# Performance work log

Hardware: AMD Instinct MI355X
Metric: run time of the kernel (lower is better)

The kernel has to match this reference:

```python
import jax, jax.numpy as jnp
import numpy as np

N = 100000
E = 1600000
F1 = 512
F3 = 128
H = 128
C = 64
SW = 0.2
FW = 1.0 - SW
BN_EPS = 1e-5


def setup_inputs() -> dict:
    key = jax.random.key(0)
    ks = jax.random.split(key, 12)
    def glorot(k, shape):
        lim = float(np.sqrt(6.0 / (shape[0] + shape[1])))
        return jax.random.uniform(k, shape, jnp.float32, -lim, lim)
    return {
        "x1": jax.random.normal(ks[0], (N, F1), jnp.float32),
        "x2": jax.random.normal(ks[1], (N, F3), jnp.float32),
        "edge_index": jax.random.randint(ks[2], (2, E), 0, N, jnp.int64),
        "W1": glorot(ks[3], (F1, H)), "b1": jnp.zeros((H,), jnp.float32),
        "W2": glorot(ks[4], (F3, H)), "b2": jnp.zeros((H,), jnp.float32),
        "Wg1": glorot(ks[5], (H, H)), "bg1": jnp.zeros((H,), jnp.float32),
        "Wg2": glorot(ks[6], (H, C)), "bg2": jnp.zeros((C,), jnp.float32),
        "gamma": jnp.ones((H,), jnp.float32), "beta": jnp.zeros((H,), jnp.float32),
        "rmean": jnp.zeros((H,), jnp.float32), "rvar": jnp.ones((H,), jnp.float32),
    }


def reference(x1, x2, edge_index, W1, b1, W2, b2, Wg1, bg1, Wg2, bg2, gamma, beta, rmean, rvar):
    # Embedding blend: fw * lin1(features) + sw * lin2(structural embedding)
    h = FW * (x1 @ W1 + b1) + SW * (x2 @ W2 + b2)  # [N, H]
    src, dst = edge_index[0], edge_index[1]
    # GCNConv layer 1 (normalize=False, add_self_loops=False): transform then scatter-add
    z = h @ Wg1                                              # [N, H]
    agg = jax.ops.segment_sum(z[src], dst, num_segments=N) + bg1  # [N, H]
    # BatchNorm1d (eval, running stats) + ReLU; dropout is identity in eval
    agg = (agg - rmean) * jax.lax.rsqrt(rvar + BN_EPS) * gamma + beta
    agg = jax.nn.relu(agg)
    # GCNConv layer 2 -> logits
    z2 = agg @ Wg2                                           # [N, C]
    out = jax.ops.segment_sum(z2[src], dst, num_segments=N) + bg2
    return out
```

## Files before the change

### kernel.cpp

```cpp
#include <hip/hip_runtime.h>
#include <hip/hip_fp16.h>
#include <cstddef>

#define NN    100000
#define EE    1600000
#define F1D   512
#define F3D   128
#define HD    128
#define CD    64
#define SWc   0.2f
#define FWc   0.8f
#define BN_EPS 1e-5f

#define SCAN_B 1024
#define NB ((NN + SCAN_B - 1) / SCAN_B)

typedef _Float16 half8 __attribute__((ext_vector_type(8)));
typedef float f32x4 __attribute__((ext_vector_type(4)));

__global__ __launch_bounds__(256) void count_kernel(
    const int* __restrict__ dst, int* __restrict__ deg)
{
    int e = blockIdx.x * 256 + threadIdx.x;
    if (e < EE) atomicAdd(&deg[dst[e]], 1);
}

__global__ __launch_bounds__(SCAN_B) void scan_partial_kernel(
    const int* __restrict__ deg, int* __restrict__ partials)
{
    __shared__ int sh[SCAN_B / 64];
    int i = blockIdx.x * SCAN_B + threadIdx.x;
    int v = (i < NN) ? deg[i] : 0;
#pragma unroll
    for (int d = 32; d > 0; d >>= 1) v += __shfl_down(v, d, 64);
    int lane = threadIdx.x & 63, wv = threadIdx.x >> 6;
    if (lane == 0) sh[wv] = v;
    __syncthreads();
    if (threadIdx.x < SCAN_B / 64) {
        int s = sh[threadIdx.x];
#pragma unroll
        for (int d = SCAN_B / 128; d > 0; d >>= 1) s += __shfl_down(s, d, 64);
        if (threadIdx.x == 0) partials[blockIdx.x] = s;
    }
}

__global__ __launch_bounds__(128) void scan_base_kernel(
    int* __restrict__ partials, int* __restrict__ offsets)
{
    __shared__ int sh[128];
    int t = threadIdx.x;
    int v = (t < NB) ? partials[t] : 0;
    sh[t] = v;
    __syncthreads();
    for (int d = 1; d < 128; d <<= 1) {
        int u = (t >= d) ? sh[t - d] : 0;
        __syncthreads();
        sh[t] += u;
        __syncthreads();
    }
    if (t < NB) partials[t] = sh[t] - v;
    if (t == NB - 1) offsets[NN] = sh[t];
}

__global__ __launch_bounds__(SCAN_B) void scan_apply_kernel(
    const int* __restrict__ deg, const int* __restrict__ partials,
    int* __restrict__ offsets, int* __restrict__ cursor)
{
    __shared__ int sh[SCAN_B];
    int t = threadIdx.x;
    int i = blockIdx.x * SCAN_B + t;
    int v = (i < NN) ? deg[i] : 0;
    sh[t] = v;
    __syncthreads();
    for (int d = 1; d < SCAN_B; d <<= 1) {
        int u = (t >= d) ? sh[t - d] : 0;
        __syncthreads();
        sh[t] += u;
        __syncthreads();
    }
    if (i < NN) {
        int excl = sh[t] - v + partials[blockIdx.x];
        offsets[i] = excl;
        cursor[i]  = excl;
    }
}

__global__ __launch_bounds__(256) void fill_kernel(
    const int* __restrict__ src, const int* __restrict__ dst,
    int* __restrict__ cursor, int* __restrict__ csr_src)
{
    int e = blockIdx.x * 256 + threadIdx.x;
    if (e < EE) {
        int d = dst[e];
        int pos = atomicAdd(&cursor[d], 1);
        csr_src[pos] = src[e];
    }
}

__global__ __launch_bounds__(256) void prep_kernel(
    const float* __restrict__ W1, const float* __restrict__ W2,
    const float* __restrict__ Wg1, const float* __restrict__ Wg2,
    const float* __restrict__ b1, const float* __restrict__ b2,
    _Float16* __restrict__ Wc_t, _Float16* __restrict__ Wg1_t,
    _Float16* __restrict__ Wg2_t, float* __restrict__ hbuf)
{
    int i = blockIdx.x * 256 + threadIdx.x;
    if (i < 128 * 640) {
        int n = i / 640, k = i % 640;
        float v = (k < F1D) ? FWc * W1[(size_t)k * HD + n]
                            : SWc * W2[(size_t)(k - F1D) * HD + n];
        Wc_t[i] = (_Float16)v;
    } else if (i < 128 * 640 + 128 * 128) {
        int j = i - 128 * 640; int n = j / 128, k = j % 128;
        Wg1_t[j] = (_Float16)Wg1[(size_t)k * HD + n];
    } else if (i < 128 * 640 + 128 * 128 + 64 * 128) {
        int j = i - 128 * 640 - 128 * 128; int n = j / 128, k = j % 128;
        Wg2_t[j] = (_Float16)Wg2[(size_t)k * CD + n];
    } else if (i < 128 * 640 + 128 * 128 + 64 * 128 + 128) {
        int j = i - (128 * 640 + 128 * 128 + 64 * 128);
        hbuf[j] = FWc * b1[j] + SWc * b2[j];
    }
}

__global__ __launch_bounds__(256) void gemm1_mfma(
    const float* __restrict__ x1, const float* __restrict__ x2,
    const _Float16* __restrict__ Wc_t, const _Float16* __restrict__ Wg1_t,
    const float* __restrict__ hbuf, _Float16* __restrict__ z)
{
    __shared__ __align__(16) _Float16 As[128][72];
    __shared__ __align__(16) _Float16 Bs[128][72];
    __shared__ __align__(16) _Float16 Hs[128][136];

    const int tid  = threadIdx.x;
    const int wave = tid >> 6;
    const int lane = tid & 63;
    const int quad = lane >> 4;
    const int l16  = lane & 15;
    const int row0 = blockIdx.x * 128;

    const int sr = tid >> 1;
    const int sc = (tid & 1) * 32;

    f32x4 acc[2][8];
    const f32x4 zero4 = {0.f, 0.f, 0.f, 0.f};
#pragma unroll
    for (int mi = 0; mi < 2; ++mi)
#pragma unroll
        for (int ni = 0; ni < 8; ++ni) acc[mi][ni] = zero4;

    for (int t = 0; t < 10; ++t) {
        const float* xp; int stride, kb;
        if (t < 8) { xp = x1; stride = F1D; kb = t * 64; }
        else       { xp = x2; stride = F3D; kb = (t - 8) * 64; }
        __syncthreads();
        {
            int gr = row0 + sr;
            if (gr < NN) {
                const float4* rp = (const float4*)(xp + (size_t)gr * stride + kb + sc);
#pragma unroll
                for (int i = 0; i < 4; ++i) {
                    float4 f0 = rp[2 * i];
                    float4 f1 = rp[2 * i + 1];
                    half8 hv = { (_Float16)f0.x, (_Float16)f0.y, (_Float16)f0.z, (_Float16)f0.w,
                                 (_Float16)f1.x, (_Float16)f1.y, (_Float16)f1.z, (_Float16)f1.w };
                    *(half8*)&As[sr][sc + i * 8] = hv;
                }
            } else {
                half8 zv = { (_Float16)0.f, (_Float16)0.f, (_Float16)0.f, (_Float16)0.f,
                             (_Float16)0.f, (_Float16)0.f, (_Float16)0.f, (_Float16)0.f };
#pragma unroll
                for (int i = 0; i < 4; ++i) *(half8*)&As[sr][sc + i * 8] = zv;
            }
            const _Float16* wp = Wc_t + (size_t)sr * 640 + t * 64 + sc;
#pragma unroll
            for (int i = 0; i < 4; ++i)
                *(half8*)&Bs[sr][sc + i * 8] = *(const half8*)(wp + i * 8);
        }
        __syncthreads();
#pragma unroll
        for (int ks = 0; ks < 2; ++ks) {
            half8 a[2], b[8];
#pragma unroll
            for (int mi = 0; mi < 2; ++mi)
                a[mi] = *(const half8*)&As[wave * 32 + mi * 16 + l16][ks * 32 + quad * 8];
#pragma unroll
            for (int ni = 0; ni < 8; ++ni)
                b[ni] = *(const half8*)&Bs[ni * 16 + l16][ks * 32 + quad * 8];
#pragma unroll
            for (int mi = 0; mi < 2; ++mi)
#pragma unroll
                for (int ni = 0; ni < 8; ++ni)
                    acc[mi][ni] = __builtin_amdgcn_mfma_f32_16x16x32_f16(
                        a[mi], b[ni], acc[mi][ni], 0, 0, 0);
        }
    }

    {
        float hbv[8];
#pragma unroll
        for (int ni = 0; ni < 8; ++ni) hbv[ni] = hbuf[ni * 16 + l16];
#pragma unroll
        for (int mi = 0; mi < 2; ++mi)
#pragma unroll
            for (int ni = 0; ni < 8; ++ni)
#pragma unroll
                for (int r = 0; r < 4; ++r)
                    Hs[wave * 32 + mi * 16 + quad * 4 + r][ni * 16 + l16] =
                        (_Float16)(acc[mi][ni][r] + hbv[ni]);
    }

#pragma unroll
    for (int mi = 0; mi < 2; ++mi)
#pragma unroll
        for (int ni = 0; ni < 8; ++ni) acc[mi][ni] = zero4;

    for (int t = 0; t < 2; ++t) {
        __syncthreads();
        {
            const _Float16* wp = Wg1_t + (size_t)sr * 128 + t * 64 + sc;
#pragma unroll
            for (int i = 0; i < 4; ++i)
                *(half8*)&Bs[sr][sc + i * 8] = *(const half8*)(wp + i * 8);
        }
        __syncthreads();
#pragma unroll
        for (int ks = 0; ks < 2; ++ks) {
            half8 a[2], b[8];
#pragma unroll
            for (int mi = 0; mi < 2; ++mi)
                a[mi] = *(const half8*)&Hs[wave * 32 + mi * 16 + l16][t * 64 + ks * 32 + quad * 8];
#pragma unroll
            for (int ni = 0; ni < 8; ++ni)
                b[ni] = *(const half8*)&Bs[ni * 16 + l16][ks * 32 + quad * 8];
#pragma unroll
            for (int mi = 0; mi < 2; ++mi)
#pragma unroll
                for (int ni = 0; ni < 8; ++ni)
                    acc[mi][ni] = __builtin_amdgcn_mfma_f32_16x16x32_f16(
                        a[mi], b[ni], acc[mi][ni], 0, 0, 0);
        }
    }

#pragma unroll
    for (int mi = 0; mi < 2; ++mi)
#pragma unroll
        for (int ni = 0; ni < 8; ++ni)
#pragma unroll
            for (int r = 0; r < 4; ++r)
                Hs[wave * 32 + mi * 16 + quad * 4 + r][ni * 16 + l16] =
                    (_Float16)acc[mi][ni][r];
    __syncthreads();
    {
        int gr = row0 + sr;
        if (gr < NN) {
            int c0 = (tid & 1) * 64;
            _Float16* zp = z + (size_t)gr * HD + c0;
#pragma unroll
            for (int i = 0; i < 8; ++i)
                *(half8*)(zp + i * 8) = *(const half8*)&Hs[sr][c0 + i * 8];
        }
    }
}

__global__ __launch_bounds__(256) void gemm2_mfma(
    const float* __restrict__ agg, const _Float16* __restrict__ Wg2_t,
    const float* __restrict__ bg1, const float* __restrict__ gamma,
    const float* __restrict__ beta, const float* __restrict__ rmean,
    const float* __restrict__ rvar, _Float16* __restrict__ z2)
{
    __shared__ __align__(16) _Float16 As[128][72];
    __shared__ __align__(16) _Float16 Bs[64][72];
    __shared__ float sS[HD], sT[HD];

    const int tid = threadIdx.x;
    if (tid < HD) {
        float s = gamma[tid] * rsqrtf(rvar[tid] + BN_EPS);
        sS[tid] = s;
        sT[tid] = (bg1[tid] - rmean[tid]) * s + beta[tid];
    }
    __syncthreads();

    const int wave = tid >> 6;
    const int lane = tid & 63;
    const int quad = lane >> 4;
    const int l16  = lane & 15;
    const int row0 = blockIdx.x * 128;
    const int sr = tid >> 1;
    const int sc = (tid & 1) * 32;

    f32x4 acc[2][4];
    const f32x4 zero4 = {0.f, 0.f, 0.f, 0.f};
#pragma unroll
    for (int mi = 0; mi < 2; ++mi)
#pragma unroll
        for (int ni = 0; ni < 4; ++ni) acc[mi][ni] = zero4;

    for (int t = 0; t < 2; ++t) {
        __syncthreads();
        {
            int gr = row0 + sr;
            if (gr < NN) {
                const float4* rp = (const float4*)(agg + (size_t)gr * HD + t * 64 + sc);
#pragma unroll
                for (int i = 0; i < 4; ++i) {
                    float4 f0 = rp[2 * i];
                    float4 f1 = rp[2 * i + 1];
                    int k = t * 64 + sc + i * 8;
                    float v0 = fmaxf(fmaf(f0.x, sS[k + 0], sT[k + 0]), 0.f);
                    float v1 = fmaxf(fmaf(f0.y, sS[k + 1], sT[k + 1]), 0.f);
                    float v2 = fmaxf(fmaf(f0.z, sS[k + 2], sT[k + 2]), 0.f);
                    float v3 = fmaxf(fmaf(f0.w, sS[k + 3], sT[k + 3]), 0.f);
                    float v4 = fmaxf(fmaf(f1.x, sS[k + 4], sT[k + 4]), 0.f);
                    float v5 = fmaxf(fmaf(f1.y, sS[k + 5], sT[k + 5]), 0.f);
                    float v6 = fmaxf(fmaf(f1.z, sS[k + 6], sT[k + 6]), 0.f);
                    float v7 = fmaxf(fmaf(f1.w, sS[k + 7], sT[k + 7]), 0.f);
                    half8 hv = { (_Float16)v0, (_Float16)v1, (_Float16)v2, (_Float16)v3,
                                 (_Float16)v4, (_Float16)v5, (_Float16)v6, (_Float16)v7 };
                    *(half8*)&As[sr][sc + i * 8] = hv;
                }
            } else {
                half8 zv = { (_Float16)0.f, (_Float16)0.f, (_Float16)0.f, (_Float16)0.f,
                             (_Float16)0.f, (_Float16)0.f, (_Float16)0.f, (_Float16)0.f };
#pragma unroll
                for (int i = 0; i < 4; ++i) *(half8*)&As[sr][sc + i * 8] = zv;
            }
            int n = tid >> 2, c = (tid & 3) * 16;
            const _Float16* wp = Wg2_t + (size_t)n * 128 + t * 64 + c;
            *(half8*)&Bs[n][c]     = *(const half8*)wp;
            *(half8*)&Bs[n][c + 8] = *(const half8*)(wp + 8);
        }
        __syncthreads();
#pragma unroll
        for (int ks = 0; ks < 2; ++ks) {
            half8 a[2], b[4];
#pragma unroll
            for (int mi = 0; mi < 2; ++mi)
                a[mi] = *(const half8*)&As[wave * 32 + mi * 16 + l16][ks * 32 + quad * 8];
#pragma unroll
            for (int ni = 0; ni < 4; ++ni)
                b[ni] = *(const half8*)&Bs[ni * 16 + l16][ks * 32 + quad * 8];
#pragma unroll
            for (int mi = 0; mi < 2; ++mi)
#pragma unroll
                for (int ni = 0; ni < 4; ++ni)
                    acc[mi][ni] = __builtin_amdgcn_mfma_f32_16x16x32_f16(
                        a[mi], b[ni], acc[mi][ni], 0, 0, 0);
        }
    }

    __syncthreads();
#pragma unroll
    for (int mi = 0; mi < 2; ++mi)
#pragma unroll
        for (int ni = 0; ni < 4; ++ni)
#pragma unroll
            for (int r = 0; r < 4; ++r)
                As[wave * 32 + mi * 16 + quad * 4 + r][ni * 16 + l16] =
                    (_Float16)acc[mi][ni][r];
    __syncthreads();
    {
        int gr = row0 + sr;
        if (gr < NN) {
            _Float16* zp = z2 + (size_t)gr * CD + sc;
            *(half8*)(zp)      = *(const half8*)&As[sr][sc];
            *(half8*)(zp + 8)  = *(const half8*)&As[sr][sc + 8];
            *(half8*)(zp + 16) = *(const half8*)&As[sr][sc + 16];
            *(half8*)(zp + 24) = *(const half8*)&As[sr][sc + 24];
        }
    }
}

__global__ __launch_bounds__(256) void gather1_kernel(
    const _Float16* __restrict__ z, const int* __restrict__ offsets,
    const int* __restrict__ csr_src, float* __restrict__ agg)
{
    int node = blockIdx.x * 4 + (threadIdx.x >> 6);
    if (node >= NN) return;
    const int lane = threadIdx.x & 63;
    const int h  = lane >> 4;
    const int fl = lane & 15;

    int beg = offsets[node];
    int cnt = offsets[node + 1] - beg;

    float a0 = 0.f, a1 = 0.f, a2 = 0.f, a3 = 0.f;
    float a4 = 0.f, a5 = 0.f, a6 = 0.f, a7 = 0.f;

    for (int j0 = 0; j0 < cnt; j0 += 64) {
        int cntc = cnt - j0; if (cntc > 64) cntc = 64;
        int myidx = (lane < cntc) ? csr_src[beg + j0 + lane] : 0;
        int nq = (cntc + 3) >> 2;
#pragma unroll 4
        for (int i = 0; i < nq; ++i) {
            int e = i * 4 + h;
            int si = __shfl(myidx, e);
            float m = (e < cntc) ? 1.f : 0.f;
            float4 raw = *(const float4*)(z + (size_t)si * HD + fl * 8);
            const __half2* hp = (const __half2*)&raw;
            float2 f0 = __half22float2(hp[0]);
            float2 f1 = __half22float2(hp[1]);
            float2 f2 = __half22float2(hp[2]);
            float2 f3 = __half22float2(hp[3]);
            a0 = fmaf(m, f0.x, a0); a1 = fmaf(m, f0.y, a1);
            a2 = fmaf(m, f1.x, a2); a3 = fmaf(m, f1.y, a3);
            a4 = fmaf(m, f2.x, a4); a5 = fmaf(m, f2.y, a5);
            a6 = fmaf(m, f3.x, a6); a7 = fmaf(m, f3.y, a7);
        }
    }

    a0 += __shfl_xor(a0, 16); a1 += __shfl_xor(a1, 16);
    a2 += __shfl_xor(a2, 16); a3 += __shfl_xor(a3, 16);
    a4 += __shfl_xor(a4, 16); a5 += __shfl_xor(a5, 16);
    a6 += __shfl_xor(a6, 16); a7 += __shfl_xor(a7, 16);
    a0 += __shfl_xor(a0, 32); a1 += __shfl_xor(a1, 32);
    a2 += __shfl_xor(a2, 32); a3 += __shfl_xor(a3, 32);
    a4 += __shfl_xor(a4, 32); a5 += __shfl_xor(a5, 32);
    a6 += __shfl_xor(a6, 32); a7 += __shfl_xor(a7, 32);

    if (h == 0) {
        float* op = agg + (size_t)node * HD + fl * 8;
        float4 o0 = make_float4(a0, a1, a2, a3);
        float4 o1 = make_float4(a4, a5, a6, a7);
        *(float4*)op       = o0;
        *(float4*)(op + 4) = o1;
    }
}

__global__ __launch_bounds__(256) void gather2_kernel(
    const _Float16* __restrict__ z2, const int* __restrict__ offsets,
    const int* __restrict__ csr_src, const float* __restrict__ bg2,
    float* __restrict__ out)
{
    int node = blockIdx.x * 4 + (threadIdx.x >> 6);
    if (node >= NN) return;
    const int lane = threadIdx.x & 63;
    const int h  = lane >> 4;
    const int fl = lane & 15;

    int beg = offsets[node];
    int cnt = offsets[node + 1] - beg;

    float a0 = 0.f, a1 = 0.f, a2 = 0.f, a3 = 0.f;

    for (int j0 = 0; j0 < cnt; j0 += 64) {
        int cntc = cnt - j0; if (cntc > 64) cntc = 64;
        int myidx = (lane < cntc) ? csr_src[beg + j0 + lane] : 0;
        int nq = (cntc + 3) >> 2;
#pragma unroll 4
        for (int i = 0; i < nq; ++i) {
            int e = i * 4 + h;
            int si = __shfl(myidx, e);
            float m = (e < cntc) ? 1.f : 0.f;
            float2 raw = *(const float2*)(z2 + (size_t)si * CD + fl * 4);
            const __half2* hp = (const __half2*)&raw;
            float2 f0 = __half22float2(hp[0]);
            float2 f1 = __half22float2(hp[1]);
            a0 = fmaf(m, f0.x, a0); a1 = fmaf(m, f0.y, a1);
            a2 = fmaf(m, f1.x, a2); a3 = fmaf(m, f1.y, a3);
        }
    }

    a0 += __shfl_xor(a0, 16); a1 += __shfl_xor(a1, 16);
    a2 += __shfl_xor(a2, 16); a3 += __shfl_xor(a3, 16);
    a0 += __shfl_xor(a0, 32); a1 += __shfl_xor(a1, 32);
    a2 += __shfl_xor(a2, 32); a3 += __shfl_xor(a3, 32);

    if (h == 0) {
        float4 bv = *(const float4*)(bg2 + fl * 4);
        float4 o = make_float4(a0 + bv.x, a1 + bv.y, a2 + bv.z, a3 + bv.w);
        *(float4*)(out + (size_t)node * CD + fl * 4) = o;
    }
}

extern "C" void kernel_launch(void* const* d_in, const int* in_sizes, int n_in,
                              void* d_out, int out_size, void* d_ws, size_t ws_size,
                              hipStream_t stream)
{
    const float* x1    = (const float*)d_in[0];
    const float* x2    = (const float*)d_in[1];
    const int*   ei    = (const int*)d_in[2];
    const float* W1    = (const float*)d_in[3];
    const float* b1    = (const float*)d_in[4];
    const float* W2    = (const float*)d_in[5];
    const float* b2    = (const float*)d_in[6];
    const float* Wg1   = (const float*)d_in[7];
    const float* bg1   = (const float*)d_in[8];
    const float* Wg2   = (const float*)d_in[9];
    const float* bg2   = (const float*)d_in[10];
    const float* gamma = (const float*)d_in[11];
    const float* beta  = (const float*)d_in[12];
    const float* rmean = (const float*)d_in[13];
    const float* rvar  = (const float*)d_in[14];
    float* out = (float*)d_out;

    char* p = (char*)d_ws;
    _Float16* z_h  = (_Float16*)p; p += (size_t)NN * HD * sizeof(_Float16);
    float*  agg    = (float*)p;    p += (size_t)NN * HD * sizeof(float);
    int*    csr    = (int*)p;      p += (size_t)EE * sizeof(int);
    int*    offs   = (int*)p;      p += (size_t)(NN + 16) * sizeof(int);
    int*    curs   = (int*)p;      p += (size_t)(NN + 16) * sizeof(int);
    int*    deg    = (int*)p;      p += (size_t)(NN + 16) * sizeof(int);
    int*    parts  = (int*)p;      p += (size_t)(NB + 16) * sizeof(int);
    _Float16* Wc_t = (_Float16*)p; p += (size_t)128 * 640 * sizeof(_Float16);
    _Float16* Wg1t = (_Float16*)p; p += (size_t)128 * 128 * sizeof(_Float16);
    _Float16* Wg2t = (_Float16*)p; p += (size_t)64 * 128 * sizeof(_Float16);
    float*  hbuf   = (float*)p;    p += 128 * sizeof(float);
    _Float16* z2_h = z_h;

    const int* src = ei;
    const int* dst = ei + EE;

    prep_kernel<<<(128 * 640 + 128 * 128 + 64 * 128 + 128 + 255) / 256, 256, 0, stream>>>(
        W1, W2, Wg1, Wg2, b1, b2, Wc_t, Wg1t, Wg2t, hbuf);

    hipMemsetAsync(deg, 0, (size_t)NN * sizeof(int), stream);
    count_kernel<<<(EE + 255) / 256, 256, 0, stream>>>(dst, deg);
    scan_partial_kernel<<<NB, SCAN_B, 0, stream>>>(deg, parts);
    scan_base_kernel<<<1, 128, 0, stream>>>(parts, offs);
    scan_apply_kernel<<<NB, SCAN_B, 0, stream>>>(deg, parts, offs, curs);
    fill_kernel<<<(EE + 255) / 256, 256, 0, stream>>>(src, dst, curs, csr);

    gemm1_mfma<<<(NN + 127) / 128, 256, 0, stream>>>(x1, x2, Wc_t, Wg1t, hbuf, z_h);
    gather1_kernel<<<(NN + 3) / 4, 256, 0, stream>>>(z_h, offs, csr, agg);
    gemm2_mfma<<<(NN + 127) / 128, 256, 0, stream>>>(agg, Wg2t, bg1, gamma, beta,
                                                     rmean, rvar, z2_h);
    gather2_kernel<<<(NN + 3) / 4, 256, 0, stream>>>(z2_h, offs, csr, bg2, out);
}
```

Baseline: 688.2 us.

## Build CSR via two-pass bucketed counting sort instead of global atomic fill

Replaces the per-edge global atomic scatter into CSR with a two-level sort. Edges are first binned by destination bucket of 128 nodes, using shared-memory histograms and one global atomic per bucket per chunk. Each bucket is then placed into its final CSR slots with shared-memory atomics and coalesced writes. The goal is to cut random global atomics and scattered writes, at the cost of two extra kernels and an intermediate buffer aliased onto agg.

```diff
diff --git a/kernel.cpp b/kernel.cpp
--- a/kernel.cpp
+++ b/kernel.cpp
@@ -15,6 +15,12 @@
 #define SCAN_B 1024
 #define NB ((NN + SCAN_B - 1) / SCAN_B)
 
+#define BSH   7
+#define NBKA  1024
+#define NBUK  ((NN + 127) / 128)
+#define CHK   4096
+#define BCAP  8192
+
 typedef _Float16 half8 __attribute__((ext_vector_type(8)));
 typedef float f32x4 __attribute__((ext_vector_type(4)));
 
@@ -85,15 +91,108 @@
     }
 }
 
-__global__ __launch_bounds__(256) void fill_kernel(
+__global__ __launch_bounds__(256) void binit_kernel(
+    const int* __restrict__ offsets, int* __restrict__ gcur)
+{
+    int b = blockIdx.x * 256 + threadIdx.x;
+    if (b < NBKA) {
+        int n = b << BSH;
+        if (n > NN) n = NN;
+        gcur[b] = offsets[n];
+    }
+}
+
+__global__ __launch_bounds__(256) void bucket_kernel(
     const int* __restrict__ src, const int* __restrict__ dst,
-    int* __restrict__ cursor, int* __restrict__ csr_src)
-{
-    int e = blockIdx.x * 256 + threadIdx.x;
-    if (e < EE) {
-        int d = dst[e];
-        int pos = atomicAdd(&cursor[d], 1);
-        csr_src[pos] = src[e];
+    int* __restrict__ gcur, int* __restrict__ ebuf)
+{
+    __shared__ int hist[NBKA];
+    __shared__ int gb2[NBKA];
+    __shared__ int tsum[256];
+    __shared__ int stage[CHK];
+    __shared__ int destg[CHK];
+
+    const int t  = threadIdx.x;
+    const int e0 = blockIdx.x * CHK;
+    int ecnt = EE - e0;
+    if (ecnt > CHK) ecnt = CHK;
+
+    for (int b = t; b < NBKA; b += 256) hist[b] = 0;
+    __syncthreads();
+
+    for (int i = t; i < ecnt; i += 256) {
+        int d = dst[e0 + i];
+        atomicAdd(&hist[d >> BSH], 1);
+    }
+    __syncthreads();
+
+    int a0 = hist[4 * t], a1 = hist[4 * t + 1];
+    int a2 = hist[4 * t + 2], a3 = hist[4 * t + 3];
+    int tot = a0 + a1 + a2 + a3;
+    tsum[t] = tot;
+    __syncthreads();
+    for (int d = 1; d < 256; d <<= 1) {
+        int u = (t >= d) ? tsum[t - d] : 0;
+        __syncthreads();
+        tsum[t] += u;
+        __syncthreads();
+    }
+    int base = tsum[t] - tot;
+    int o0 = base, o1 = base + a0, o2 = base + a0 + a1, o3 = base + a0 + a1 + a2;
+    if (a0 > 0) gb2[4 * t]     = atomicAdd(&gcur[4 * t],     a0) - o0;
+    if (a1 > 0) gb2[4 * t + 1] = atomicAdd(&gcur[4 * t + 1], a1) - o1;
+    if (a2 > 0) gb2[4 * t + 2] = atomicAdd(&gcur[4 * t + 2], a2) - o2;
+    if (a3 > 0) gb2[4 * t + 3] = atomicAdd(&gcur[4 * t + 3], a3) - o3;
+    hist[4 * t] = o0; hist[4 * t + 1] = o1;
+    hist[4 * t + 2] = o2; hist[4 * t + 3] = o3;
+    __syncthreads();
+
+    for (int i = t; i < ecnt; i += 256) {
+        int d = dst[e0 + i];
+        int s = src[e0 + i];
+        int b = d >> BSH;
+        int pos = atomicAdd(&hist[b], 1);
+        stage[pos] = (s << BSH) | (d & 127);
+        destg[pos] = gb2[b] + pos;
+    }
+    __syncthreads();
+
+    for (int sx = t; sx < ecnt; sx += 256) ebuf[destg[sx]] = stage[sx];
+}
+
+__global__ __launch_bounds__(256) void csr_place_kernel(
+    const int* __restrict__ ebuf, const int* __restrict__ offsets,
+    int* __restrict__ cursor, int* __restrict__ csr)
+{
+    __shared__ int lcur[128];
+    __shared__ int stage[BCAP];
+
+    const int b   = blockIdx.x;
+    const int t   = threadIdx.x;
+    const int nb0 = b << BSH;
+    int nb1 = nb0 + 128;
+    if (nb1 > NN) nb1 = NN;
+    const int rbeg = offsets[nb0];
+    const int rend = offsets[nb1];
+    const int L = rend - rbeg;
+
+    if (L <= BCAP) {
+        if (t < nb1 - nb0) lcur[t] = offsets[nb0 + t] - rbeg;
+        __syncthreads();
+        for (int e = rbeg + t; e < rend; e += 256) {
+            int p = ebuf[e];
+            int pos = atomicAdd(&lcur[p & 127], 1);
+            stage[pos] = p >> BSH;
+        }
+        __syncthreads();
+        for (int s = t; s < L; s += 256) csr[rbeg + s] = stage[s];
+    } else {
+        for (int e = rbeg + t; e < rend; e += 256) {
+            int p = ebuf[e];
+            int node = nb0 + (p & 127);
+            int pos = atomicAdd(&cursor[node], 1);
+            csr[pos] = p >> BSH;
+        }
     }
 }
 
@@ -501,11 +600,13 @@
     int*    curs   = (int*)p;      p += (size_t)(NN + 16) * sizeof(int);
     int*    deg    = (int*)p;      p += (size_t)(NN + 16) * sizeof(int);
     int*    parts  = (int*)p;      p += (size_t)(NB + 16) * sizeof(int);
+    int*    gcur   = (int*)p;      p += (size_t)(NBKA + 16) * sizeof(int);
     _Float16* Wc_t = (_Float16*)p; p += (size_t)128 * 640 * sizeof(_Float16);
     _Float16* Wg1t = (_Float16*)p; p += (size_t)128 * 128 * sizeof(_Float16);
     _Float16* Wg2t = (_Float16*)p; p += (size_t)64 * 128 * sizeof(_Float16);
     float*  hbuf   = (float*)p;    p += 128 * sizeof(float);
     _Float16* z2_h = z_h;
+    int*    ebuf   = (int*)agg;
 
     const int* src = ei;
     const int* dst = ei + EE;
@@ -518,7 +619,9 @@
     scan_partial_kernel<<<NB, SCAN_B, 0, stream>>>(deg, parts);
     scan_base_kernel<<<1, 128, 0, stream>>>(parts, offs);
     scan_apply_kernel<<<NB, SCAN_B, 0, stream>>>(deg, parts, offs, curs);
-    fill_kernel<<<(EE + 255) / 256, 256, 0, stream>>>(src, dst, curs, csr);
+    binit_kernel<<<(NBKA + 255) / 256, 256, 0, stream>>>(offs, gcur);
+    bucket_kernel<<<(EE + CHK - 1) / CHK, 256, 0, stream>>>(src, dst, gcur, ebuf);
+    csr_place_kernel<<<NBUK, 256, 0, stream>>>(ebuf, offs, curs, csr);
 
     gemm1_mfma<<<(NN + 127) / 128, 256, 0, stream>>>(x1, x2, Wc_t, Wg1t, hbuf, z_h);
     gather1_kernel<<<(NN + 3) / 4, 256, 0, stream>>>(z_h, offs, csr, agg);
```

After: 641.2 us. -6.8%, faster.
